# Kernel optimization log

Measured on AMD Instinct MI355X. Metric: run time of the kernel, lower is better.

Reference implementation:

```python
import jax, jax.numpy as jnp
import numpy as np

B, F, CTX, HID, L, NB = 16384, 64, 128, 512, 8, 2


def setup_inputs() -> dict:
    key = jax.random.key(0)
    ks = jax.random.split(key, 8)
    inputs = jax.random.normal(ks[0], (B, F), jnp.float32)
    context = jax.random.normal(ks[1], (B, CTX), jnp.float32)
    n_id = F // 2                      # identity features per coupling layer
    in_dim = n_id + CTX                # coupling net input = identity half + context
    out_dim = F                        # 2 * num_transform_features (shift | scale)
    s_in = 1.0 / np.sqrt(in_dim)
    s_h = 1.0 / np.sqrt(HID)
    W_in = jax.random.uniform(ks[2], (L, in_dim, HID), jnp.float32, -s_in, s_in)
    b_in = jax.random.uniform(ks[3], (L, HID), jnp.float32, -s_in, s_in)
    W_h = jax.random.uniform(ks[4], (L, NB, HID, HID), jnp.float32, -s_h, s_h)
    b_h = jax.random.uniform(ks[5], (L, NB, HID), jnp.float32, -s_h, s_h)
    # output layer init: normal(0, 0.01) weight, zero bias (as in torch source)
    W_out = 0.01 * jax.random.normal(ks[6], (L, HID, out_dim), jnp.float32)
    b_out = jnp.zeros((L, out_dim), jnp.float32)
    # fixed random permutations between coupling layers (nflows RandomPermutation buffers)
    rng = np.random.RandomState(42)
    perms = jnp.asarray(np.stack([rng.permutation(F) for _ in range(L - 1)]), jnp.int32)
    return dict(inputs=inputs, context=context, W_in=W_in, b_in=b_in,
                W_h=W_h, b_h=b_h, W_out=W_out, b_out=b_out, perms=perms)


def reference(inputs, context, W_in, b_in, W_h, b_h, W_out, b_out, perms):
    F_ = inputs.shape[-1]
    n_layers = W_in.shape[0]
    n_blocks = W_h.shape[1]
    nt = F_ // 2  # num transform features
    even_idx = jnp.arange(0, F_, 2)
    odd_idx = jnp.arange(1, F_, 2)
    x = jnp.clip(inputs, -1.0, 1.0)
    logdet = jnp.zeros(x.shape[0], x.dtype)
    for i in range(n_layers):
        # mask[::2]=1 for even layers -> mask>0 (even indices) are TRANSFORM features
        if i % 2 == 0:
            t_idx, id_idx = even_idx, odd_idx
        else:
            t_idx, id_idx = odd_idx, even_idx
        id_split = x[:, id_idx]   # [B, nt]
        tr_split = x[:, t_idx]    # [B, nt]
        h = jax.nn.relu(jnp.concatenate([id_split, context], -1) @ W_in[i] + b_in[i])
        for j in range(n_blocks):
            h = jax.nn.relu(h @ W_h[i, j] + b_h[i, j])
        p = h @ W_out[i] + b_out[i]            # [B, 2*nt]
        shift = p[:, :nt]
        scale = jax.nn.sigmoid(p[:, nt:] + 2.0) + 1e-3
        logdet = logdet + jnp.sum(jnp.log(scale), axis=-1)
        x = x.at[:, t_idx].set(tr_split * scale + shift).at[:, id_idx].set(id_split)
        if i < n_layers - 1:
            x = x[:, perms[i]]
    return jnp.clip(x, -1.0, 1.0), logdet
```

## Files before the change

kernel.cpp:

```cpp
#include <hip/hip_runtime.h>


typedef float v4f  __attribute__((ext_vector_type(4)));
typedef float v16f __attribute__((ext_vector_type(16)));
typedef int   v4i  __attribute__((ext_vector_type(4)));
typedef int   v8i  __attribute__((ext_vector_type(8)));
typedef unsigned char uchar;
typedef unsigned long long ull;

#define BATCH 16384
#define NF    64
#define NCTX  128
#define NL    8

#define RS     528
#define HHALF  256
#define AST    208
#define AHALF  96

#define WSCALE     16.0f
#define WSCALE_INV 0.0625f

#define WIN_EPL   (192 * 512)
#define WH_EPB    (512 * 512)
#define WOUT_EPL  (512 * 64)
#define OFF_WIN   ((size_t)0)
#define OFF_WH    ((size_t)(8 * WIN_EPL))
#define OFF_WOUT  (OFF_WH + (size_t)(16 * WH_EPB))
#define TOT_PACK_ELEMS (OFF_WOUT + (size_t)(8 * WOUT_EPL))
#define NEED_WS   (TOT_PACK_ELEMS)

#define NU_IN   192
#define NU_H    1024
#define NU_OUT  128
#define NU_TOT  (NU_IN + NU_H + NU_OUT)

template<bool HI>
__device__ __forceinline__ unsigned int pk2(float a, float b, unsigned int old) {
    return __builtin_amdgcn_cvt_pk_fp8_f32(a, b, old, HI);
}
__device__ __forceinline__ uchar q8(float v) {
    return (uchar)(__builtin_amdgcn_cvt_pk_fp8_f32(v, v, 0u, false) & 0xffu);
}

__device__ __forceinline__ void bar_lds() {
    asm volatile("s_waitcnt lgkmcnt(0)" ::: "memory");
    __builtin_amdgcn_s_barrier();
    asm volatile("" ::: "memory");
}

__global__ __launch_bounds__(256) void pack_weights_kernel(
    const float* __restrict__ W_in,
    const float* __restrict__ W_h,
    const float* __restrict__ W_out,
    unsigned char* __restrict__ ws) {
    const int wid  = (blockIdx.x * blockDim.x + threadIdx.x) >> 6;
    const int lane = threadIdx.x & 63;
    if (wid >= NU_TOT) return;

    if (wid < NU_IN + NU_H) {
        const float* src;
        uchar* dstbase;
        int kb, khalf, g, rawK;
        if (wid < NU_IN) {
            int i = wid / 24, r = wid % 24;
            kb = r >> 3; khalf = (r >> 2) & 1; g = r & 3;
            src = W_in + (size_t)i * (160 * 512); rawK = 160;
            dstbase = ws + OFF_WIN + (size_t)i * WIN_EPL + kb * 32768;
        } else {
            int u = wid - NU_IN;
            int ij = u >> 6, r = u & 63;
            kb = r >> 3; khalf = (r >> 2) & 1; g = r & 3;
            src = W_h + (size_t)ij * WH_EPB; rawK = 512;
            dstbase = ws + OFF_WH + (size_t)ij * WH_EPB + kb * 32768;
        }
        const int pig = (g == 1) ? 2 : (g == 2) ? 1 : g;
        const int k0  = kb * 64 + khalf * 32 + pig * 8;
        const int n0  = lane * 8;
        float v[8][8];
        if (k0 < rawK) {
#pragma unroll
            for (int j = 0; j < 8; ++j) {
                const float* p = src + (size_t)(k0 + j) * 512 + n0;
                float4 a = ((const float4*)p)[0];
                float4 b = ((const float4*)p)[1];
                v[j][0] = a.x * WSCALE; v[j][1] = a.y * WSCALE;
                v[j][2] = a.z * WSCALE; v[j][3] = a.w * WSCALE;
                v[j][4] = b.x * WSCALE; v[j][5] = b.y * WSCALE;
                v[j][6] = b.z * WSCALE; v[j][7] = b.w * WSCALE;
            }
        } else {
#pragma unroll
            for (int j = 0; j < 8; ++j)
#pragma unroll
                for (int nn = 0; nn < 8; ++nn) v[j][nn] = 0.f;
        }
        uchar* dst = dstbase +
            ((lane >> 2) * 64 + 32 * khalf + (lane & 3) * 8) * 32 + g * 8;
#pragma unroll
        for (int nn = 0; nn < 8; ++nn) {
            uint2 o;
            o.x = pk2<false>(v[0][nn], v[1][nn], 0u);
            o.x = pk2<true >(v[2][nn], v[3][nn], o.x);
            o.y = pk2<false>(v[4][nn], v[5][nn], 0u);
            o.y = pk2<true >(v[6][nn], v[7][nn], o.y);
            *(uint2*)(dst + nn * 32) = o;
        }
    } else {
        int u = wid - (NU_IN + NU_H);
        int i = u >> 4, kc = u & 15;
        const float* src = W_out + (size_t)i * WOUT_EPL;
        float v[32];
#pragma unroll
        for (int k = 0; k < 32; ++k)
            v[k] = src[(size_t)(kc * 32 + k) * 64 + lane] * WSCALE;
        uchar* dst = ws + OFF_WOUT + (size_t)i * 32768 +
                     (size_t)(kc * 4 + (lane >> 4)) * 512;
#pragma unroll
        for (int ks = 0; ks < 4; ++ks) {
            uint2 o;
            o.x = pk2<false>(v[ks * 8 + 0], v[ks * 8 + 1], 0u);
            o.x = pk2<true >(v[ks * 8 + 2], v[ks * 8 + 3], o.x);
            o.y = pk2<false>(v[ks * 8 + 4], v[ks * 8 + 5], 0u);
            o.y = pk2<true >(v[ks * 8 + 6], v[ks * 8 + 7], o.y);
            *(uint2*)(dst + (ks * 16 + (lane & 15)) * 8) = o;
        }
    }
}

__device__ __forceinline__ v16f mfma32(ull a, ull b, v16f c) {
    return __builtin_amdgcn_mfma_f32_32x32x16_fp8_fp8((long)a, (long)b, c, 0, 0, 0);
}
__device__ __forceinline__ v4f mfma16(ull a, ull b, v4f c) {
    return __builtin_amdgcn_mfma_f32_16x16x32_fp8_fp8((long)a, (long)b, c, 0, 0, 0);
}
__device__ __forceinline__ v16f mfma64(v8i a, v8i b, v16f c) {
    return __builtin_amdgcn_mfma_scale_f32_32x32x64_f8f6f4(
        a, b, c, 0, 0, 0, 0x7f7f7f7f, 0, 0x7f7f7f7f);
}

__device__ __forceinline__ v8i ldv8(const uchar* p) {
    v4i lo = *(const v4i*)p;
    v4i hi = *(const v4i*)(p + 16);
    return __builtin_shufflevector(lo, hi, 0, 1, 2, 3, 4, 5, 6, 7);
}

struct BPre  { v8i b00, b10, b01, b11; };
struct BPre16 { ull u0, u1, u2, u3, v0, v1, v2, v3; } ;

__device__ __forceinline__ BPre prefB(const uchar* __restrict__ wpk,
                                      int pair, int lane) {
    const uchar* bp = wpk + (size_t)(pair * 128 + lane) * 32;
    BPre r;
    r.b00 = ldv8(bp);
    r.b10 = ldv8(bp + 2048);
    r.b01 = ldv8(bp + 32768);
    r.b11 = ldv8(bp + 32768 + 2048);
    return r;
}
__device__ __forceinline__ BPre16 prefB16(const uchar* __restrict__ wpk,
                                          int w, int lane) {
    const int npair = w & 1;
    const uchar* bp0 = wpk + (size_t)(npair * 64 + lane) * 8;
    const uchar* bp1 = wpk + (size_t)((npair + 2) * 64 + lane) * 8;
    BPre16 r;
    r.u0 = *(const ull*)(bp0);        r.u1 = *(const ull*)(bp0 + 2048);
    r.u2 = *(const ull*)(bp0 + 4096); r.u3 = *(const ull*)(bp0 + 6144);
    r.v0 = *(const ull*)(bp1);        r.v1 = *(const ull*)(bp1 + 2048);
    r.v2 = *(const ull*)(bp1 + 4096); r.v3 = *(const ull*)(bp1 + 6144);
    return r;
}

template<int NKB>
__device__ __forceinline__ void gemm32mx(
    const uchar* __restrict__ wpk,
    const float* __restrict__ bias,
    const uchar* __restrict__ Abuf, int ast, int halfoff,
    uchar* __restrict__ Obuf,
    int pair, int lane, BPre pre)
{
    const int l31 = lane & 31, hl = lane >> 5;
    v16f a00, a01, a10, a11;
#pragma unroll
    for (int r = 0; r < 16; ++r) { a00[r] = 0.f; a01[r] = 0.f;
                                   a10[r] = 0.f; a11[r] = 0.f; }
    const uchar* aLo0 = Abuf + l31 * ast + hl * 16;
    const uchar* aHi0 = aLo0 + halfoff;
    const uchar* aLo1 = aLo0 + 32 * ast;
    const uchar* aHi1 = aHi0 + 32 * ast;
    const uchar* bp = wpk + (size_t)(pair * 128 + lane) * 32;

    auto loadB = [&](int s, int kb) -> v8i {
        if (kb >= NKB) kb = NKB - 1;
        return ldv8(bp + s * 2048 + (size_t)kb * 32768);
    };
    auto loadA = [&](const uchar* lo_, const uchar* hi_, int kb) -> v8i {
        if (kb >= NKB) kb = NKB - 1;
        v4i lo = *(const v4i*)(lo_ + kb * 32);
        v4i hi = *(const v4i*)(hi_ + kb * 32);
        return __builtin_shufflevector(lo, hi, 0, 1, 2, 3, 4, 5, 6, 7);
    };

    v8i xA0 = loadA(aLo0, aHi0, 0), xA1 = loadA(aLo1, aHi1, 0);
    v8i xB0 = loadA(aLo0, aHi0, 1), xB1 = loadA(aLo1, aHi1, 1);
    v8i b00 = pre.b00, b10 = pre.b10;
    v8i b01 = pre.b01, b11 = pre.b11;
#pragma unroll 1
    for (int kb = 0; kb + 1 < NKB; kb += 2) {
        a00 = mfma64(b00, xA0, a00);
        a01 = mfma64(b00, xA1, a01);
        a10 = mfma64(b10, xA0, a10);
        a11 = mfma64(b10, xA1, a11);
        xA0 = loadA(aLo0, aHi0, kb + 2);
        xA1 = loadA(aLo1, aHi1, kb + 2);
        b00 = loadB(0, kb + 2);
        b10 = loadB(1, kb + 2);
        a00 = mfma64(b01, xB0, a00);
        a01 = mfma64(b01, xB1, a01);
        a10 = mfma64(b11, xB0, a10);
        a11 = mfma64(b11, xB1, a11);
        xB0 = loadA(aLo0, aHi0, kb + 3);
        xB1 = loadA(aLo1, aHi1, kb + 3);
        b01 = loadB(0, kb + 3);
        b11 = loadB(1, kb + 3);
    }
    if constexpr (NKB & 1) {
        a00 = mfma64(b00, xA0, a00);
        a01 = mfma64(b00, xA1, a01);
        a10 = mfma64(b10, xA0, a10);
        a11 = mfma64(b10, xA1, a11);
    }

    const uchar* ob0 = Obuf + l31 * RS + 4 * hl;
    const uchar* ob1 = ob0 + 32 * RS;
    auto emit = [&](const v16f& am0, const v16f& am1, int strip) {
#pragma unroll
        for (int q = 0; q < 4; ++q) {
            const int n0 = strip * 32 + q * 8 + 4 * hl;
            float4 bv = *(const float4*)(bias + n0);
            unsigned int u0, u1;
            u0 = pk2<false>(fmaxf(fmaf(am0[4 * q + 0], WSCALE_INV, bv.x), 0.f),
                            fmaxf(fmaf(am0[4 * q + 1], WSCALE_INV, bv.y), 0.f), 0u);
            u0 = pk2<true >(fmaxf(fmaf(am0[4 * q + 2], WSCALE_INV, bv.z), 0.f),
                            fmaxf(fmaf(am0[4 * q + 3], WSCALE_INV, bv.w), 0.f), u0);
            u1 = pk2<false>(fmaxf(fmaf(am1[4 * q + 0], WSCALE_INV, bv.x), 0.f),
                            fmaxf(fmaf(am1[4 * q + 1], WSCALE_INV, bv.y), 0.f), 0u);
            u1 = pk2<true >(fmaxf(fmaf(am1[4 * q + 2], WSCALE_INV, bv.z), 0.f),
                            fmaxf(fmaf(am1[4 * q + 3], WSCALE_INV, bv.w), 0.f), u1);
            const int g = strip * 4 + q;
            const int off = (g & 1) * HHALF + ((g >> 1) << 3);
            *(unsigned int*)(ob0 + off) = u0;
            *(unsigned int*)(ob1 + off) = u1;
        }
    };
    emit(a00, a01, pair * 2 + 0);
    emit(a10, a11, pair * 2 + 1);
}

template<int KC>
__device__ __forceinline__ void gemm32_raw(
    const float* __restrict__ wraw,
    const float* __restrict__ bias,
    const uchar* __restrict__ Abuf, int ast, int ahalf,
    uchar* __restrict__ Obuf,
    int strip, int lane)
{
    constexpr int P = KC / 2;
    const int l31 = lane & 31, hl = lane >> 5;
    v16f acc0, acc1;
#pragma unroll
    for (int r = 0; r < 16; ++r) { acc0[r] = 0.f; acc1[r] = 0.f; }
    const uchar* a0p = Abuf + l31 * ast + hl * ahalf;
    const uchar* a1p = a0p + 32 * ast;

    auto loadB = [&](int kc) -> ull {
        if (kc >= KC) kc = KC - 1;
        int n  = strip * 32 + l31;
        int k0 = kc * 16 + hl * 8;
        unsigned int lo, hi;
        lo = pk2<false>(wraw[(size_t)(k0 + 0) * 512 + n] * WSCALE,
                        wraw[(size_t)(k0 + 1) * 512 + n] * WSCALE, 0u);
        lo = pk2<true >(wraw[(size_t)(k0 + 2) * 512 + n] * WSCALE,
                        wraw[(size_t)(k0 + 3) * 512 + n] * WSCALE, lo);
        hi = pk2<false>(wraw[(size_t)(k0 + 4) * 512 + n] * WSCALE,
                        wraw[(size_t)(k0 + 5) * 512 + n] * WSCALE, 0u);
        hi = pk2<true >(wraw[(size_t)(k0 + 6) * 512 + n] * WSCALE,
                        wraw[(size_t)(k0 + 7) * 512 + n] * WSCALE, hi);
        return ((ull)hi << 32) | (ull)lo;
    };

    ull b0 = loadB(0), b1 = loadB(1), b2 = loadB(2), b3 = loadB(3);
    int p2 = 0;
#pragma unroll 1
    for (; p2 + 1 < P; p2 += 2) {
        ulonglong2 Aa0 = *(const ulonglong2*)(a0p + p2 * 16);
        ulonglong2 Aa1 = *(const ulonglong2*)(a1p + p2 * 16);
        acc0 = mfma32(Aa0.x, b0, acc0);
        acc1 = mfma32(Aa1.x, b0, acc1);
        b0 = loadB(2 * p2 + 4);
        acc0 = mfma32(Aa0.y, b1, acc0);
        acc1 = mfma32(Aa1.y, b1, acc1);
        b1 = loadB(2 * p2 + 5);
        ulonglong2 Ab0 = *(const ulonglong2*)(a0p + p2 * 16 + 16);
        ulonglong2 Ab1 = *(const ulonglong2*)(a1p + p2 * 16 + 16);
        acc0 = mfma32(Ab0.x, b2, acc0);
        acc1 = mfma32(Ab1.x, b2, acc1);
        b2 = loadB(2 * p2 + 6);
        acc0 = mfma32(Ab0.y, b3, acc0);
        acc1 = mfma32(Ab1.y, b3, acc1);
        b3 = loadB(2 * p2 + 7);
    }
    if constexpr (P & 1) {
        ulonglong2 Aa0 = *(const ulonglong2*)(a0p + (P - 1) * 16);
        ulonglong2 Aa1 = *(const ulonglong2*)(a1p + (P - 1) * 16);
        acc0 = mfma32(Aa0.x, b0, acc0);
        acc1 = mfma32(Aa1.x, b0, acc1);
        acc0 = mfma32(Aa0.y, b1, acc0);
        acc1 = mfma32(Aa1.y, b1, acc1);
    }

    const int n = strip * 32 + l31;
    const int nb = ((n >> 3) & 1) * HHALF + ((n >> 4) << 3) + (n & 7);
    const float bv = bias[n];
#pragma unroll
    for (int reg = 0; reg < 16; ++reg) {
        int row = (reg & 3) + 8 * (reg >> 2) + 4 * hl;
        float v0 = fmaxf(fmaf(acc0[reg], WSCALE_INV, bv), 0.f);
        Obuf[row * RS + nb] = q8(v0);
        float v1 = fmaxf(fmaf(acc1[reg], WSCALE_INV, bv), 0.f);
        Obuf[(row + 32) * RS + nb] = q8(v1);
    }
}

template<bool PACKED>
__device__ __forceinline__ float gemm16_fused(
    const uchar* __restrict__ wpk,
    const float* __restrict__ wraw,
    const float* __restrict__ bias,
    const uchar* __restrict__ Abuf,
    float* __restrict__ xbuf,
    const int* __restrict__ ct,
    int par, int w, int lane, BPre16 pre)
{
    const int quad = lane >> 4, l15 = lane & 15;
    const int mtb  = w >> 1;
    const int npair = w & 1;
    const int ntb0 = npair, ntb1 = npair + 2;
    const int row  = mtb * 16 + l15;
    v4f acc0, acc1;
    acc0[0] = acc0[1] = acc0[2] = acc0[3] = 0.f;
    acc1[0] = acc1[1] = acc1[2] = acc1[3] = 0.f;
    const uchar* ap = Abuf + row * RS + (quad & 1) * HHALF + ((quad >> 1) << 3);
    const uchar* bp0 =
        PACKED ? wpk + (size_t)(ntb0 * 64 + lane) * 8 : (const uchar*)0;
    const uchar* bp1 =
        PACKED ? wpk + (size_t)(ntb1 * 64 + lane) * 8 : (const uchar*)0;
    constexpr int KC = 16;

    auto loadB = [&](const uchar* bp, int ntb, int kc) -> ull {
        if (kc >= KC) kc = KC - 1;
        if constexpr (PACKED) {
            return *(const ull*)(bp + (size_t)kc * 2048);
        } else {
            int n  = ntb * 16 + l15;
            int k0 = kc * 32 + quad * 8;
            unsigned int lo, hi;
            lo = pk2<false>(wraw[(size_t)(k0 + 0) * 64 + n] * WSCALE,
                            wraw[(size_t)(k0 + 1) * 64 + n] * WSCALE, 0u);
            lo = pk2<true >(wraw[(size_t)(k0 + 2) * 64 + n] * WSCALE,
                            wraw[(size_t)(k0 + 3) * 64 + n] * WSCALE, lo);
            hi = pk2<false>(wraw[(size_t)(k0 + 4) * 64 + n] * WSCALE,
                            wraw[(size_t)(k0 + 5) * 64 + n] * WSCALE, 0u);
            hi = pk2<true >(wraw[(size_t)(k0 + 6) * 64 + n] * WSCALE,
                            wraw[(size_t)(k0 + 7) * 64 + n] * WSCALE, hi);
            return ((ull)hi << 32) | (ull)lo;
        }
    };
    auto rdA = [&](int kc) -> ull {
        if (kc >= KC) kc = KC - 1;
        return *(const ull*)(ap + kc * 16);
    };

    ull a0 = rdA(0), a1 = rdA(1), a2 = rdA(2), a3 = rdA(3);
    ull u0, u1, u2, u3, v0, v1, v2, v3;
    if constexpr (PACKED) {
        u0 = pre.u0; u1 = pre.u1; u2 = pre.u2; u3 = pre.u3;
        v0 = pre.v0; v1 = pre.v1; v2 = pre.v2; v3 = pre.v3;
    } else {
        u0 = loadB(bp0, ntb0, 0); u1 = loadB(bp0, ntb0, 1);
        u2 = loadB(bp0, ntb0, 2); u3 = loadB(bp0, ntb0, 3);
        v0 = loadB(bp1, ntb1, 0); v1 = loadB(bp1, ntb1, 1);
        v2 = loadB(bp1, ntb1, 2); v3 = loadB(bp1, ntb1, 3);
    }
    int kc = 0;
#pragma unroll 1
    for (; kc + 3 < KC; kc += 4) {
        acc0 = mfma16(u0, a0, acc0); acc1 = mfma16(v0, a0, acc1);
        a0 = rdA(kc + 4);
        u0 = loadB(bp0, ntb0, kc + 4); v0 = loadB(bp1, ntb1, kc + 4);
        acc0 = mfma16(u1, a1, acc0); acc1 = mfma16(v1, a1, acc1);
        a1 = rdA(kc + 5);
        u1 = loadB(bp0, ntb0, kc + 5); v1 = loadB(bp1, ntb1, kc + 5);
        acc0 = mfma16(u2, a2, acc0); acc1 = mfma16(v2, a2, acc1);
        a2 = rdA(kc + 6);
        u2 = loadB(bp0, ntb0, kc + 6); v2 = loadB(bp1, ntb1, kc + 6);
        acc0 = mfma16(u3, a3, acc0); acc1 = mfma16(v3, a3, acc1);
        a3 = rdA(kc + 7);
        u3 = loadB(bp0, ntb0, kc + 7); v3 = loadB(bp1, ntb1, kc + 7);
    }

    const int n0 = ntb0 * 16 + quad * 4;
    float ld = 0.f;
#pragma unroll
    for (int r = 0; r < 4; ++r) {
        float shiftv = fmaf(acc0[r], WSCALE_INV, bias[n0 + r]);
        float z      = fmaf(acc1[r], WSCALE_INV, bias[32 + n0 + r]) + 2.0f;
        float s      = 1.0f / (1.0f + __expf(-z)) + 0.001f;
        int sc = n0 + r;
        int tc = ct[2 * sc + par];
        float xo = xbuf[row * NF + tc];
        xbuf[row * NF + tc] = xo * s + shiftv;
        ld += __logf(s);
    }
    return ld;
}

template<bool PACKED>
__global__ __launch_bounds__(512, 2) void flow_kernel(
    const float* __restrict__ inputs,
    const float* __restrict__ ctx,
    const float* __restrict__ W_in,  const float* __restrict__ b_in,
    const float* __restrict__ W_h,   const float* __restrict__ b_h,
    const float* __restrict__ W_out, const float* __restrict__ b_out,
    const int*   __restrict__ perms,
    const uchar* __restrict__ wpk,
    float* __restrict__ out)
{
    __shared__ __align__(16) uchar hbuf0[64 * RS];
    __shared__ __align__(16) uchar hbuf1[64 * RS];
    __shared__ __align__(16) uchar abuf[64 * AST];
    __shared__ __align__(16) float xbuf[64 * NF];
    __shared__ int Ctab[NL * NF];

    const int tid  = threadIdx.x;
    const int wave = tid >> 6;
    const int lane = tid & 63;
    const int trow = tid >> 3;
    const int t8   = tid & 7;
    const int row0 = blockIdx.x * 64;

    {
        int i = tid >> 6, c = tid & 63;
        int idx = c;
        for (int k = i - 1; k >= 0; --k) idx = perms[k * NF + idx];
        Ctab[tid] = idx;
    }
    {
#pragma unroll
        for (int j = 0; j < 2; ++j) {
            float4 v = ((const float4*)(inputs + (size_t)row0 * NF))[tid + j * 512];
            v.x = fminf(fmaxf(v.x, -1.f), 1.f);
            v.y = fminf(fmaxf(v.y, -1.f), 1.f);
            v.z = fminf(fmaxf(v.z, -1.f), 1.f);
            v.w = fminf(fmaxf(v.w, -1.f), 1.f);
            ((float4*)xbuf)[tid + j * 512] = v;
        }
    }
    {
        const float* crow = ctx + (size_t)(row0 + trow) * NCTX + t8 * 16;
        float4 f0 = ((const float4*)crow)[0];
        float4 f1 = ((const float4*)crow)[1];
        float4 f2 = ((const float4*)crow)[2];
        float4 f3 = ((const float4*)crow)[3];
        uint2 ck0, ck1;
        ck0.x = pk2<false>(f0.x, f0.y, 0u);
        ck0.x = pk2<true >(f0.z, f0.w, ck0.x);
        ck0.y = pk2<false>(f1.x, f1.y, 0u);
        ck0.y = pk2<true >(f1.z, f1.w, ck0.y);
        ck1.x = pk2<false>(f2.x, f2.y, 0u);
        ck1.x = pk2<true >(f2.z, f2.w, ck1.x);
        ck1.y = pk2<false>(f3.x, f3.y, 0u);
        ck1.y = pk2<true >(f3.z, f3.w, ck1.y);
        *(uint2*)(abuf + trow * AST + (2 + t8) * 8) = ck0;
        *(uint2*)(abuf + trow * AST + AHALF + (2 + t8) * 8) = ck1;
    }
    if (tid < 256) {
        int r = tid >> 2, q = tid & 3;
        *(ull*)(abuf + r * AST + (q & 1) * AHALF + 80 + ((q >> 1) << 3)) = 0ULL;
    }
    float ld_acc = 0.f;

    BPre preN;
    if constexpr (PACKED) preN = prefB(wpk + OFF_WIN, wave, lane);
    bar_lds();

#pragma unroll 1
    for (int i = 0; i < NL; ++i) {
        const int par = i & 1;
        const int idp = par ^ 1;
        const int* ct = Ctab + i * NF;

        if (t8 < 4) {
            const float* xr = xbuf + trow * NF;
            uint2 idv;
            idv.x = pk2<false>(xr[ct[2 * (t8 * 8 + 0) + idp]],
                               xr[ct[2 * (t8 * 8 + 1) + idp]], 0u);
            idv.x = pk2<true >(xr[ct[2 * (t8 * 8 + 2) + idp]],
                               xr[ct[2 * (t8 * 8 + 3) + idp]], idv.x);
            idv.y = pk2<false>(xr[ct[2 * (t8 * 8 + 4) + idp]],
                               xr[ct[2 * (t8 * 8 + 5) + idp]], 0u);
            idv.y = pk2<true >(xr[ct[2 * (t8 * 8 + 6) + idp]],
                               xr[ct[2 * (t8 * 8 + 7) + idp]], idv.y);
            *(uint2*)(abuf + trow * AST + (t8 & 1) * AHALF + ((t8 >> 1) << 3)) = idv;
        }
        bar_lds();

        if constexpr (PACKED) {
            const uchar* wg1 = wpk + OFF_WH + (size_t)(i * 2 + 0) * WH_EPB;
            const uchar* wg2 = wpk + OFF_WH + (size_t)(i * 2 + 1) * WH_EPB;
            const uchar* wg3 = wpk + OFF_WOUT + (size_t)i * WOUT_EPL;
            gemm32mx<3>(wpk + OFF_WIN + (size_t)i * WIN_EPL, b_in + i * 512,
                        abuf, AST, AHALF, hbuf0, wave, lane, preN);
            BPre pre1 = prefB(wg1, wave, lane);
            bar_lds();
            gemm32mx<8>(wg1, b_h + (i * 2 + 0) * 512,
                        hbuf0, RS, HHALF, hbuf1, wave, lane, pre1);
            BPre pre2 = prefB(wg2, wave, lane);
            bar_lds();
            gemm32mx<8>(wg2, b_h + (i * 2 + 1) * 512,
                        hbuf1, RS, HHALF, hbuf0, wave, lane, pre2);
            BPre16 pre3 = prefB16(wg3, wave, lane);
            bar_lds();
            ld_acc += gemm16_fused<true>(
                wg3, W_out + (size_t)i * WOUT_EPL, b_out + i * 64,
                hbuf0, xbuf, ct, par, wave, lane, pre3);
            preN = prefB(wpk + OFF_WIN + (size_t)((i + 1) & 7) * WIN_EPL,
                         wave, lane);
            bar_lds();
        } else {
            gemm32_raw<10>(W_in + (size_t)i * (160 * 512), b_in + i * 512,
                           abuf, AST, AHALF, hbuf0, wave * 2 + 0, lane);
            gemm32_raw<10>(W_in + (size_t)i * (160 * 512), b_in + i * 512,
                           abuf, AST, AHALF, hbuf0, wave * 2 + 1, lane);
            bar_lds();
            gemm32_raw<32>(W_h + (size_t)(i * 2 + 0) * WH_EPB,
                           b_h + (i * 2 + 0) * 512,
                           hbuf0, RS, HHALF, hbuf1, wave * 2 + 0, lane);
            gemm32_raw<32>(W_h + (size_t)(i * 2 + 0) * WH_EPB,
                           b_h + (i * 2 + 0) * 512,
                           hbuf0, RS, HHALF, hbuf1, wave * 2 + 1, lane);
            bar_lds();
            gemm32_raw<32>(W_h + (size_t)(i * 2 + 1) * WH_EPB,
                           b_h + (i * 2 + 1) * 512,
                           hbuf1, RS, HHALF, hbuf0, wave * 2 + 0, lane);
            gemm32_raw<32>(W_h + (size_t)(i * 2 + 1) * WH_EPB,
                           b_h + (i * 2 + 1) * 512,
                           hbuf1, RS, HHALF, hbuf0, wave * 2 + 1, lane);
            bar_lds();
            BPre16 dummy{};
            ld_acc += gemm16_fused<false>(
                (const uchar*)0, W_out + (size_t)i * WOUT_EPL, b_out + i * 64,
                hbuf0, xbuf, ct, par, wave, lane, dummy);
            bar_lds();
        }
    }

    {
        const int* c7 = Ctab + 7 * NF;
#pragma unroll
        for (int j = 0; j < 2; ++j) {
            int p = tid + j * 512;
            int r = p >> 4, c0 = (p & 15) * 4;
            const float* xr = xbuf + r * NF;
            float4 v;
            v.x = fminf(fmaxf(xr[c7[c0 + 0]], -1.f), 1.f);
            v.y = fminf(fmaxf(xr[c7[c0 + 1]], -1.f), 1.f);
            v.z = fminf(fmaxf(xr[c7[c0 + 2]], -1.f), 1.f);
            v.w = fminf(fmaxf(xr[c7[c0 + 3]], -1.f), 1.f);
            ((float4*)(out + (size_t)row0 * NF))[p] = v;
        }
    }
    {
        float* lbuf = (float*)abuf;
        const int rrow = (wave >> 1) * 16 + (lane & 15);
        const int slot = (wave & 1) * 4 + (lane >> 4);
        lbuf[rrow * 8 + slot] = ld_acc;
        bar_lds();
        if (tid < 64) {
            float s = 0.f;
#pragma unroll
            for (int k = 0; k < 8; ++k) s += lbuf[tid * 8 + k];
            out[(size_t)BATCH * NF + row0 + tid] = s;
        }
    }
}

extern "C" void kernel_launch(void* const* d_in, const int* in_sizes, int n_in,
                              void* d_out, int out_size, void* d_ws, size_t ws_size,
                              hipStream_t stream) {
    const float* inputs  = (const float*)d_in[0];
    const float* context = (const float*)d_in[1];
    const float* W_in    = (const float*)d_in[2];
    const float* b_in    = (const float*)d_in[3];
    const float* W_h     = (const float*)d_in[4];
    const float* b_h     = (const float*)d_in[5];
    const float* W_out   = (const float*)d_in[6];
    const float* b_out   = (const float*)d_in[7];
    const int*   perms   = (const int*)d_in[8];
    float* out = (float*)d_out;

    if (ws_size >= (size_t)NEED_WS) {
        uchar* ws = (uchar*)d_ws;
        const int total_threads = NU_TOT * 64;
        pack_weights_kernel<<<(total_threads + 255) / 256, 256, 0, stream>>>(
            W_in, W_h, W_out, ws);
        flow_kernel<true><<<256, 512, 0, stream>>>(
            inputs, context, W_in, b_in, W_h, b_h, W_out, b_out, perms, ws, out);
    } else {
        flow_kernel<false><<<256, 512, 0, stream>>>(
            inputs, context, W_in, b_in, W_h, b_h, W_out, b_out, perms,
            (const uchar*)0, out);
    }
}
```

Baseline: 194.5 us.

## Halve rows per block to 32 and double occupancy to four blocks per CU

Each block now processes 32 batch rows instead of 64. Each wave keeps one M-tile of accumulators instead of two, and LDS buffers shrink. Launch bounds rise to 4 blocks per CU and the grid grows to 512 blocks, so the 256 CUs are fully used and latency is better hidden. The trade-off is that each weight fragment is reused over half as many rows, doubling per-row weight traffic from L2, and only 4 of the 8 waves take part in the output GEMM.

```diff
diff --git a/kernel.cpp b/kernel.cpp
--- a/kernel.cpp
+++ b/kernel.cpp
@@ -12,6 +12,7 @@
 #define NF    64
 #define NCTX  128
 #define NL    8
+#define ROWS  32
 
 #define RS     528
 #define HHALF  256
@@ -146,7 +147,7 @@
 }
 
 struct BPre  { v8i b00, b10, b01, b11; };
-struct BPre16 { ull u0, u1, u2, u3, v0, v1, v2, v3; } ;
+struct BPre16 { ull u0, u1, u2, u3, v0, v1, v2, v3; };
 
 __device__ __forceinline__ BPre prefB(const uchar* __restrict__ wpk,
                                       int pair, int lane) {
@@ -180,81 +181,63 @@
     int pair, int lane, BPre pre)
 {
     const int l31 = lane & 31, hl = lane >> 5;
-    v16f a00, a01, a10, a11;
-#pragma unroll
-    for (int r = 0; r < 16; ++r) { a00[r] = 0.f; a01[r] = 0.f;
-                                   a10[r] = 0.f; a11[r] = 0.f; }
-    const uchar* aLo0 = Abuf + l31 * ast + hl * 16;
-    const uchar* aHi0 = aLo0 + halfoff;
-    const uchar* aLo1 = aLo0 + 32 * ast;
-    const uchar* aHi1 = aHi0 + 32 * ast;
+    v16f a00, a10;
+#pragma unroll
+    for (int r = 0; r < 16; ++r) { a00[r] = 0.f; a10[r] = 0.f; }
+    const uchar* aLo = Abuf + l31 * ast + hl * 16;
+    const uchar* aHi = aLo + halfoff;
     const uchar* bp = wpk + (size_t)(pair * 128 + lane) * 32;
 
     auto loadB = [&](int s, int kb) -> v8i {
         if (kb >= NKB) kb = NKB - 1;
         return ldv8(bp + s * 2048 + (size_t)kb * 32768);
     };
-    auto loadA = [&](const uchar* lo_, const uchar* hi_, int kb) -> v8i {
+    auto loadA = [&](int kb) -> v8i {
         if (kb >= NKB) kb = NKB - 1;
-        v4i lo = *(const v4i*)(lo_ + kb * 32);
-        v4i hi = *(const v4i*)(hi_ + kb * 32);
+        v4i lo = *(const v4i*)(aLo + kb * 32);
+        v4i hi = *(const v4i*)(aHi + kb * 32);
         return __builtin_shufflevector(lo, hi, 0, 1, 2, 3, 4, 5, 6, 7);
     };
 
-    v8i xA0 = loadA(aLo0, aHi0, 0), xA1 = loadA(aLo1, aHi1, 0);
-    v8i xB0 = loadA(aLo0, aHi0, 1), xB1 = loadA(aLo1, aHi1, 1);
+    v8i xA = loadA(0), xB = loadA(1);
     v8i b00 = pre.b00, b10 = pre.b10;
     v8i b01 = pre.b01, b11 = pre.b11;
 #pragma unroll 1
     for (int kb = 0; kb + 1 < NKB; kb += 2) {
-        a00 = mfma64(b00, xA0, a00);
-        a01 = mfma64(b00, xA1, a01);
-        a10 = mfma64(b10, xA0, a10);
-        a11 = mfma64(b10, xA1, a11);
-        xA0 = loadA(aLo0, aHi0, kb + 2);
-        xA1 = loadA(aLo1, aHi1, kb + 2);
+        a00 = mfma64(b00, xA, a00);
+        a10 = mfma64(b10, xA, a10);
+        xA = loadA(kb + 2);
         b00 = loadB(0, kb + 2);
         b10 = loadB(1, kb + 2);
-        a00 = mfma64(b01, xB0, a00);
-        a01 = mfma64(b01, xB1, a01);
-        a10 = mfma64(b11, xB0, a10);
-        a11 = mfma64(b11, xB1, a11);
-        xB0 = loadA(aLo0, aHi0, kb + 3);
-        xB1 = loadA(aLo1, aHi1, kb + 3);
+        a00 = mfma64(b01, xB, a00);
+        a10 = mfma64(b11, xB, a10);
+        xB = loadA(kb + 3);
         b01 = loadB(0, kb + 3);
         b11 = loadB(1, kb + 3);
     }
     if constexpr (NKB & 1) {
-        a00 = mfma64(b00, xA0, a00);
-        a01 = mfma64(b00, xA1, a01);
-        a10 = mfma64(b10, xA0, a10);
-        a11 = mfma64(b10, xA1, a11);
-    }
-
-    const uchar* ob0 = Obuf + l31 * RS + 4 * hl;
-    const uchar* ob1 = ob0 + 32 * RS;
-    auto emit = [&](const v16f& am0, const v16f& am1, int strip) {
+        a00 = mfma64(b00, xA, a00);
+        a10 = mfma64(b10, xA, a10);
+    }
+
+    const uchar* ob = Obuf + l31 * RS + 4 * hl;
+    auto emit = [&](const v16f& am, int strip) {
 #pragma unroll
         for (int q = 0; q < 4; ++q) {
             const int n0 = strip * 32 + q * 8 + 4 * hl;
             float4 bv = *(const float4*)(bias + n0);
-            unsigned int u0, u1;
-            u0 = pk2<false>(fmaxf(fmaf(am0[4 * q + 0], WSCALE_INV, bv.x), 0.f),
-                            fmaxf(fmaf(am0[4 * q + 1], WSCALE_INV, bv.y), 0.f), 0u);
-            u0 = pk2<true >(fmaxf(fmaf(am0[4 * q + 2], WSCALE_INV, bv.z), 0.f),
-                            fmaxf(fmaf(am0[4 * q + 3], WSCALE_INV, bv.w), 0.f), u0);
-            u1 = pk2<false>(fmaxf(fmaf(am1[4 * q + 0], WSCALE_INV, bv.x), 0.f),
-                            fmaxf(fmaf(am1[4 * q + 1], WSCALE_INV, bv.y), 0.f), 0u);
-            u1 = pk2<true >(fmaxf(fmaf(am1[4 * q + 2], WSCALE_INV, bv.z), 0.f),
-                            fmaxf(fmaf(am1[4 * q + 3], WSCALE_INV, bv.w), 0.f), u1);
+            unsigned int u0;
+            u0 = pk2<false>(fmaxf(fmaf(am[4 * q + 0], WSCALE_INV, bv.x), 0.f),
+                            fmaxf(fmaf(am[4 * q + 1], WSCALE_INV, bv.y), 0.f), 0u);
+            u0 = pk2<true >(fmaxf(fmaf(am[4 * q + 2], WSCALE_INV, bv.z), 0.f),
+                            fmaxf(fmaf(am[4 * q + 3], WSCALE_INV, bv.w), 0.f), u0);
             const int g = strip * 4 + q;
             const int off = (g & 1) * HHALF + ((g >> 1) << 3);
-            *(unsigned int*)(ob0 + off) = u0;
-            *(unsigned int*)(ob1 + off) = u1;
+            *(unsigned int*)(ob + off) = u0;
         }
     };
-    emit(a00, a01, pair * 2 + 0);
-    emit(a10, a11, pair * 2 + 1);
+    emit(a00, pair * 2 + 0);
+    emit(a10, pair * 2 + 1);
 }
 
 template<int KC>
@@ -267,11 +250,10 @@
 {
     constexpr int P = KC / 2;
     const int l31 = lane & 31, hl = lane >> 5;
-    v16f acc0, acc1;
-#pragma unroll
-    for (int r = 0; r < 16; ++r) { acc0[r] = 0.f; acc1[r] = 0.f; }
+    v16f acc0;
+#pragma unroll
+    for (int r = 0; r < 16; ++r) acc0[r] = 0.f;
     const uchar* a0p = Abuf + l31 * ast + hl * ahalf;
-    const uchar* a1p = a0p + 32 * ast;
 
     auto loadB = [&](int kc) -> ull {
         if (kc >= KC) kc = KC - 1;
@@ -294,29 +276,20 @@
 #pragma unroll 1
     for (; p2 + 1 < P; p2 += 2) {
         ulonglong2 Aa0 = *(const ulonglong2*)(a0p + p2 * 16);
-        ulonglong2 Aa1 = *(const ulonglong2*)(a1p + p2 * 16);
         acc0 = mfma32(Aa0.x, b0, acc0);
-        acc1 = mfma32(Aa1.x, b0, acc1);
         b0 = loadB(2 * p2 + 4);
         acc0 = mfma32(Aa0.y, b1, acc0);
-        acc1 = mfma32(Aa1.y, b1, acc1);
         b1 = loadB(2 * p2 + 5);
         ulonglong2 Ab0 = *(const ulonglong2*)(a0p + p2 * 16 + 16);
-        ulonglong2 Ab1 = *(const ulonglong2*)(a1p + p2 * 16 + 16);
         acc0 = mfma32(Ab0.x, b2, acc0);
-        acc1 = mfma32(Ab1.x, b2, acc1);
         b2 = loadB(2 * p2 + 6);
         acc0 = mfma32(Ab0.y, b3, acc0);
-        acc1 = mfma32(Ab1.y, b3, acc1);
         b3 = loadB(2 * p2 + 7);
     }
     if constexpr (P & 1) {
         ulonglong2 Aa0 = *(const ulonglong2*)(a0p + (P - 1) * 16);
-        ulonglong2 Aa1 = *(const ulonglong2*)(a1p + (P - 1) * 16);
         acc0 = mfma32(Aa0.x, b0, acc0);
-        acc1 = mfma32(Aa1.x, b0, acc1);
         acc0 = mfma32(Aa0.y, b1, acc0);
-        acc1 = mfma32(Aa1.y, b1, acc1);
     }
 
     const int n = strip * 32 + l31;
@@ -327,8 +300,6 @@
         int row = (reg & 3) + 8 * (reg >> 2) + 4 * hl;
         float v0 = fmaxf(fmaf(acc0[reg], WSCALE_INV, bv), 0.f);
         Obuf[row * RS + nb] = q8(v0);
-        float v1 = fmaxf(fmaf(acc1[reg], WSCALE_INV, bv), 0.f);
-        Obuf[(row + 32) * RS + nb] = q8(v1);
     }
 }
 
@@ -426,7 +397,7 @@
 }
 
 template<bool PACKED>
-__global__ __launch_bounds__(512, 2) void flow_kernel(
+__global__ __launch_bounds__(512, 4) void flow_kernel(
     const float* __restrict__ inputs,
     const float* __restrict__ ctx,
     const float* __restrict__ W_in,  const float* __restrict__ b_in,
@@ -436,18 +407,18 @@
     const uchar* __restrict__ wpk,
     float* __restrict__ out)
 {
-    __shared__ __align__(16) uchar hbuf0[64 * RS];
-    __shared__ __align__(16) uchar hbuf1[64 * RS];
-    __shared__ __align__(16) uchar abuf[64 * AST];
-    __shared__ __align__(16) float xbuf[64 * NF];
+    __shared__ __align__(16) uchar hbuf0[ROWS * RS];
+    __shared__ __align__(16) uchar hbuf1[ROWS * RS];
+    __shared__ __align__(16) uchar abuf[ROWS * AST];
+    __shared__ __align__(16) float xbuf[ROWS * NF];
     __shared__ int Ctab[NL * NF];
 
     const int tid  = threadIdx.x;
     const int wave = tid >> 6;
     const int lane = tid & 63;
-    const int trow = tid >> 3;
-    const int t8   = tid & 7;
-    const int row0 = blockIdx.x * 64;
+    const int trow = tid >> 4;
+    const int t16  = tid & 15;
+    const int row0 = blockIdx.x * ROWS;
 
     {
         int i = tid >> 6, c = tid & 63;
@@ -456,35 +427,25 @@
         Ctab[tid] = idx;
     }
     {
-#pragma unroll
-        for (int j = 0; j < 2; ++j) {
-            float4 v = ((const float4*)(inputs + (size_t)row0 * NF))[tid + j * 512];
-            v.x = fminf(fmaxf(v.x, -1.f), 1.f);
-            v.y = fminf(fmaxf(v.y, -1.f), 1.f);
-            v.z = fminf(fmaxf(v.z, -1.f), 1.f);
-            v.w = fminf(fmaxf(v.w, -1.f), 1.f);
-            ((float4*)xbuf)[tid + j * 512] = v;
-        }
+        float4 v = ((const float4*)(inputs + (size_t)row0 * NF))[tid];
+        v.x = fminf(fmaxf(v.x, -1.f), 1.f);
+        v.y = fminf(fmaxf(v.y, -1.f), 1.f);
+        v.z = fminf(fmaxf(v.z, -1.f), 1.f);
+        v.w = fminf(fmaxf(v.w, -1.f), 1.f);
+        ((float4*)xbuf)[tid] = v;
     }
     {
-        const float* crow = ctx + (size_t)(row0 + trow) * NCTX + t8 * 16;
+        const float* crow = ctx + (size_t)(row0 + trow) * NCTX + t16 * 8;
         float4 f0 = ((const float4*)crow)[0];
         float4 f1 = ((const float4*)crow)[1];
-        float4 f2 = ((const float4*)crow)[2];
-        float4 f3 = ((const float4*)crow)[3];
-        uint2 ck0, ck1;
-        ck0.x = pk2<false>(f0.x, f0.y, 0u);
-        ck0.x = pk2<true >(f0.z, f0.w, ck0.x);
-        ck0.y = pk2<false>(f1.x, f1.y, 0u);
-        ck0.y = pk2<true >(f1.z, f1.w, ck0.y);
-        ck1.x = pk2<false>(f2.x, f2.y, 0u);
-        ck1.x = pk2<true >(f2.z, f2.w, ck1.x);
-        ck1.y = pk2<false>(f3.x, f3.y, 0u);
-        ck1.y = pk2<true >(f3.z, f3.w, ck1.y);
-        *(uint2*)(abuf + trow * AST + (2 + t8) * 8) = ck0;
-        *(uint2*)(abuf + trow * AST + AHALF + (2 + t8) * 8) = ck1;
-    }
-    if (tid < 256) {
+        uint2 ck;
+        ck.x = pk2<false>(f0.x, f0.y, 0u);
+        ck.x = pk2<true >(f0.z, f0.w, ck.x);
+        ck.y = pk2<false>(f1.x, f1.y, 0u);
+        ck.y = pk2<true >(f1.z, f1.w, ck.y);
+        *(uint2*)(abuf + trow * AST + (t16 & 1) * AHALF + (2 + (t16 >> 1)) * 8) = ck;
+    }
+    if (tid < 128) {
         int r = tid >> 2, q = tid & 3;
         *(ull*)(abuf + r * AST + (q & 1) * AHALF + 80 + ((q >> 1) << 3)) = 0ULL;
     }
@@ -500,18 +461,18 @@
         const int idp = par ^ 1;
         const int* ct = Ctab + i * NF;
 
-        if (t8 < 4) {
+        if (t16 < 4) {
             const float* xr = xbuf + trow * NF;
             uint2 idv;
-            idv.x = pk2<false>(xr[ct[2 * (t8 * 8 + 0) + idp]],
-                               xr[ct[2 * (t8 * 8 + 1) + idp]], 0u);
-            idv.x = pk2<true >(xr[ct[2 * (t8 * 8 + 2) + idp]],
-                               xr[ct[2 * (t8 * 8 + 3) + idp]], idv.x);
-            idv.y = pk2<false>(xr[ct[2 * (t8 * 8 + 4) + idp]],
-                               xr[ct[2 * (t8 * 8 + 5) + idp]], 0u);
-            idv.y = pk2<true >(xr[ct[2 * (t8 * 8 + 6) + idp]],
-                               xr[ct[2 * (t8 * 8 + 7) + idp]], idv.y);
-            *(uint2*)(abuf + trow * AST + (t8 & 1) * AHALF + ((t8 >> 1) << 3)) = idv;
+            idv.x = pk2<false>(xr[ct[2 * (t16 * 8 + 0) + idp]],
+                               xr[ct[2 * (t16 * 8 + 1) + idp]], 0u);
+            idv.x = pk2<true >(xr[ct[2 * (t16 * 8 + 2) + idp]],
+                               xr[ct[2 * (t16 * 8 + 3) + idp]], idv.x);
+            idv.y = pk2<false>(xr[ct[2 * (t16 * 8 + 4) + idp]],
+                               xr[ct[2 * (t16 * 8 + 5) + idp]], 0u);
+            idv.y = pk2<true >(xr[ct[2 * (t16 * 8 + 6) + idp]],
+                               xr[ct[2 * (t16 * 8 + 7) + idp]], idv.y);
+            *(uint2*)(abuf + trow * AST + (t16 & 1) * AHALF + ((t16 >> 1) << 3)) = idv;
         }
         bar_lds();
 
@@ -529,11 +490,12 @@
             bar_lds();
             gemm32mx<8>(wg2, b_h + (i * 2 + 1) * 512,
                         hbuf1, RS, HHALF, hbuf0, wave, lane, pre2);
-            BPre16 pre3 = prefB16(wg3, wave, lane);
-            bar_lds();
-            ld_acc += gemm16_fused<true>(
-                wg3, W_out + (size_t)i * WOUT_EPL, b_out + i * 64,
-                hbuf0, xbuf, ct, par, wave, lane, pre3);
+            BPre16 pre3 = prefB16(wg3, wave & 3, lane);
+            bar_lds();
+            if (wave < 4)
+                ld_acc += gemm16_fused<true>(
+                    wg3, W_out + (size_t)i * WOUT_EPL, b_out + i * 64,
+                    hbuf0, xbuf, ct, par, wave, lane, pre3);
             preN = prefB(wpk + OFF_WIN + (size_t)((i + 1) & 7) * WIN_EPL,
                          wave, lane);
             bar_lds();
@@ -558,35 +520,34 @@
                            hbuf1, RS, HHALF, hbuf0, wave * 2 + 1, lane);
             bar_lds();
             BPre16 dummy{};
-            ld_acc += gemm16_fused<false>(
-                (const uchar*)0, W_out + (size_t)i * WOUT_EPL, b_out + i * 64,
-                hbuf0, xbuf, ct, par, wave, lane, dummy);
+            if (wave < 4)
+                ld_acc += gemm16_fused<false>(
+                    (const uchar*)0, W_out + (size_t)i * WOUT_EPL,
+                    b_out + i * 64, hbuf0, xbuf, ct, par, wave, lane, dummy);
             bar_lds();
         }
     }
 
     {
         const int* c7 = Ctab + 7 * NF;
-#pragma unroll
-        for (int j = 0; j < 2; ++j) {
-            int p = tid + j * 512;
-            int r = p >> 4, c0 = (p & 15) * 4;
-            const float* xr = xbuf + r * NF;
-            float4 v;
-            v.x = fminf(fmaxf(xr[c7[c0 + 0]], -1.f), 1.f);
-            v.y = fminf(fmaxf(xr[c7[c0 + 1]], -1.f), 1.f);
-            v.z = fminf(fmaxf(xr[c7[c0 + 2]], -1.f), 1.f);
-            v.w = fminf(fmaxf(xr[c7[c0 + 3]], -1.f), 1.f);
-            ((float4*)(out + (size_t)row0 * NF))[p] = v;
-        }
+        int r = tid >> 4, c0 = (tid & 15) * 4;
+        const float* xr = xbuf + r * NF;
+        float4 v;
+        v.x = fminf(fmaxf(xr[c7[c0 + 0]], -1.f), 1.f);
+        v.y = fminf(fmaxf(xr[c7[c0 + 1]], -1.f), 1.f);
+        v.z = fminf(fmaxf(xr[c7[c0 + 2]], -1.f), 1.f);
+        v.w = fminf(fmaxf(xr[c7[c0 + 3]], -1.f), 1.f);
+        ((float4*)(out + (size_t)row0 * NF))[tid] = v;
     }
     {
         float* lbuf = (float*)abuf;
-        const int rrow = (wave >> 1) * 16 + (lane & 15);
-        const int slot = (wave & 1) * 4 + (lane >> 4);
-        lbuf[rrow * 8 + slot] = ld_acc;
+        if (wave < 4) {
+            const int rrow = (wave >> 1) * 16 + (lane & 15);
+            const int slot = (wave & 1) * 4 + (lane >> 4);
+            lbuf[rrow * 8 + slot] = ld_acc;
+        }
         bar_lds();
-        if (tid < 64) {
+        if (tid < ROWS) {
             float s = 0.f;
 #pragma unroll
             for (int k = 0; k < 8; ++k) s += lbuf[tid * 8 + k];
@@ -609,15 +570,17 @@
     const int*   perms   = (const int*)d_in[8];
     float* out = (float*)d_out;
 
+    const int nblocks = BATCH / ROWS;
+
     if (ws_size >= (size_t)NEED_WS) {
         uchar* ws = (uchar*)d_ws;
         const int total_threads = NU_TOT * 64;
         pack_weights_kernel<<<(total_threads + 255) / 256, 256, 0, stream>>>(
             W_in, W_h, W_out, ws);
-        flow_kernel<true><<<256, 512, 0, stream>>>(
+        flow_kernel<true><<<nblocks, 512, 0, stream>>>(
             inputs, context, W_in, b_in, W_h, b_h, W_out, b_out, perms, ws, out);
     } else {
-        flow_kernel<false><<<256, 512, 0, stream>>>(
+        flow_kernel<false><<<nblocks, 512, 0, stream>>>(
             inputs, context, W_in, b_in, W_h, b_h, W_out, b_out, perms,
             (const uchar*)0, out);
     }
```

Result: slower. 236.5 us (+21.6%).
